# Kernel optimization log

Measured on AMD Instinct MI355X. Metric: run time of the kernel, lower is better.

The kernel has to match this reference:

```python
import jax, jax.numpy as jnp
import numpy as np

T, N, DH, E = 4, 50000, 64, 800000
BN_EPS = 1e-5


def setup_inputs() -> dict:
    key = jax.random.key(0)
    ks = jax.random.split(key, 8)
    node_data = jax.random.normal(ks[0], (T, N, DH), dtype=jnp.float32)
    edge_weight = jax.random.uniform(ks[1], (E,), dtype=jnp.float32)
    W1 = jax.random.normal(ks[2], (DH, 3 * DH), dtype=jnp.float32) * 0.05
    b1 = jax.random.normal(ks[3], (DH,), dtype=jnp.float32) * 0.05
    gamma = jnp.ones((3 * DH,), dtype=jnp.float32)
    beta = jnp.zeros((3 * DH,), dtype=jnp.float32)
    src = jax.random.randint(ks[4], (E,), 0, N)
    dst = jax.random.randint(ks[5], (E,), 0, N)
    return {"node_data": node_data, "edge_weight": edge_weight, "W1": W1,
            "b1": b1, "gamma": gamma, "beta": beta, "src": src, "dst": dst}


def reference(node_data, edge_weight, W1, b1, gamma, beta, src, dst):
    # --- sparse weighted neighbor aggregation (torch.bmm with sparse ew) ---
    # msg[t, e, :] = w_e * x[t, src_e, :]
    msg = node_data[:, src, :] * edge_weight[None, :, None]          # [T, E, dh]
    agg = jnp.zeros((T, N, DH), jnp.float32).at[:, dst, :].add(msg)  # [T, N, dh]
    # Z = torch.sparse.sum(ew, dim=2); Z[Z==0]=1 (degree normalization)
    Z = jnp.zeros((N,), jnp.float32).at[dst].add(edge_weight)
    Z = jnp.where(Z == 0, 1.0, Z)
    avg_neighbor = agg / Z[None, :, None]
    # prev_state: zeros at t=0, shifted node_data otherwise
    prev = jnp.concatenate([jnp.zeros((1, N, DH), jnp.float32), node_data[:-1]], axis=0)
    inp = jnp.concatenate([node_data, prev, avg_neighbor], axis=2).reshape(T * N, 3 * DH)
    # --- ReluFCN with batchnorm (training-mode batch stats, biased var) ---
    mu = jnp.mean(inp, axis=0)
    var = jnp.mean(jnp.square(inp - mu), axis=0)
    xhat = (inp - mu) * jax.lax.rsqrt(var + BN_EPS) * gamma + beta
    out = jax.nn.relu(xhat @ W1.T + b1)
    return out.reshape(T, N, DH)
```

## Files before the change

kernel.cpp:

```cpp
#include <hip/hip_runtime.h>

#define TT 4
#define NN 50000
#define DH 64
#define EE 800000
#define BN_EPS 1e-5f
#define G1 64
#define EB 2048
#define AGG_B 2048
#define AGG_W (AGG_B*4)
#define MAIN_B 768
#define FOLD_B 8
#define CAP 32
#define DSTR 8
#define PASLOT 32
#define OVMAX 256

typedef __attribute__((ext_vector_type(8))) short short8;
typedef __attribute__((ext_vector_type(4))) float floatx4;

#define WS_PA       0
#define WS_PA2      8192
#define WS_PX       16384
#define WS_PX2      81920
#define WS_W1EFF    147456
#define WS_B1EFF    172032
#define WS_OVC      172288
#define WS_OVF      172544
#define WS_DEG      176640
#define WS_PACKED   1776640
#define WS_XB       8176640
#define WS_AVGB     33776640

__device__ __forceinline__ unsigned short f2b(float f) {
    unsigned int u = __float_as_uint(f);
    unsigned int r = (u + 0x7FFFu + ((u >> 16) & 1u)) >> 16;
    return (unsigned short)r;
}
__device__ __forceinline__ float b2f(unsigned short u) {
    return __uint_as_float((unsigned int)u << 16);
}
__device__ __forceinline__ unsigned short f2h(float f) {
    _Float16 h = (_Float16)f;
    unsigned short u; __builtin_memcpy(&u, &h, 2); return u;
}
__device__ __forceinline__ float h2f(unsigned short u) {
    _Float16 h; __builtin_memcpy(&h, &u, 2); return (float)h;
}

__global__ __launch_bounds__(256) void k_prep_stats(
    const float* __restrict__ x, unsigned short* __restrict__ xb,
    float* __restrict__ PX, float* __restrict__ PX2,
    int* __restrict__ deg, int* __restrict__ ovc) {
    int t = blockIdx.y;
    int tid = threadIdx.x;
    int gid = (t * G1 + blockIdx.x) * 256 + tid;
    int4* deg4 = (int4*)deg;
    for (int i = gid; i < NN * DSTR / 4; i += 65536)
        deg4[i] = make_int4(0, 0, 0, 0);
    if (gid == 0) *ovc = 0;

    int g = blockIdx.x * 256 + tid;
    const floatx4* xt = (const floatx4*)(x + (size_t)t * NN * 64);
    float s[4] = {0.f, 0.f, 0.f, 0.f}, s2[4] = {0.f, 0.f, 0.f, 0.f};
    for (int v = g; v < NN * 16; v += G1 * 256) {
        floatx4 d = __builtin_nontemporal_load(&xt[v]);
        ushort4 o;
        o.x = f2b(d.x); o.y = f2b(d.y); o.z = f2b(d.z); o.w = f2b(d.w);
        *(ushort4*)(xb + (size_t)(v >> 4) * 256 + t * 64 + (v & 15) * 4) = o;
        s[0] += d.x; s2[0] += d.x * d.x;
        s[1] += d.y; s2[1] += d.y * d.y;
        s[2] += d.z; s2[2] += d.z * d.z;
        s[3] += d.w; s2[3] += d.w * d.w;
    }
    __shared__ float ls[256 * 4], ls2[256 * 4];
#pragma unroll
    for (int j = 0; j < 4; ++j) { ls[tid * 4 + j] = s[j]; ls2[tid * 4 + j] = s2[j]; }
    __syncthreads();
    if (tid < 64) {
        int g16 = tid >> 2, comp = tid & 3;
        float rs = 0.f, rs2 = 0.f;
#pragma unroll
        for (int k = 0; k < 16; ++k) {
            int j = g16 + 16 * k;
            rs += ls[j * 4 + comp]; rs2 += ls2[j * 4 + comp];
        }
        int slot = (t * G1 + blockIdx.x) * 64 + tid;
        PX[slot] = rs; PX2[slot] = rs2;
    }
}

__global__ __launch_bounds__(256) void k_fillB(
    const int* __restrict__ src, const int* __restrict__ dst,
    const float* __restrict__ ew, int* __restrict__ deg,
    unsigned int* __restrict__ packed, int* __restrict__ ovc,
    int4* __restrict__ ovf, float* __restrict__ PA) {
    int gtid = blockIdx.x * 256 + threadIdx.x;
    if (gtid < 2 * PASLOT * 64) PA[gtid] = 0.f;
    for (int e = gtid; e < EE; e += EB * 256) {
        int d = dst[e];
        int s = src[e];
        float w = ew[e];
        int slot = atomicAdd(&deg[d * DSTR], 1);
        if (slot < CAP) {
            packed[d * CAP + slot] = (unsigned int)s | ((unsigned int)f2h(w) << 16);
        } else {
            int o = atomicAdd(ovc, 1);
            if (o < OVMAX) ovf[o] = make_int4(d, s, __float_as_int(w), 0);
        }
    }
}

__global__ __launch_bounds__(256) void k_agg(
    const unsigned short* __restrict__ xb, const unsigned int* __restrict__ packed,
    const int* __restrict__ deg, const int* __restrict__ ovc,
    const int4* __restrict__ ovf, unsigned short* __restrict__ avgb,
    float* __restrict__ PA, float* __restrict__ PA2) {
    int wv = __builtin_amdgcn_readfirstlane(threadIdx.x >> 6);
    int tid = threadIdx.x;
    int l = tid & 63;
    int wgid = blockIdx.x * 4 + wv;
    const ushort4* xl = (const ushort4*)xb + l;
    int nov = *ovc; nov = nov > OVMAX ? OVMAX : nov;
    float sA[4] = {0.f, 0.f, 0.f, 0.f}, sA2[4] = {0.f, 0.f, 0.f, 0.f};

    for (int n = wgid; n < NN; n += AGG_W) {
        int dg = deg[n * DSTR];
        int cnt = dg < CAP ? dg : CAP;
        const unsigned int* bkt = packed + n * CAP;
        float a0 = 0.f, a1 = 0.f, a2 = 0.f, a3 = 0.f, wsum = 0.f;
        for (int e = 0; e < cnt; e += 8) {
            int rem = cnt - e;
            unsigned int p[8];
#pragma unroll
            for (int j = 0; j < 8; ++j) p[j] = bkt[e + j];
            ushort4 v[8];
#pragma unroll
            for (int j = 0; j < 8; ++j) {
                int sidx = (j < rem) ? (int)(p[j] & 0xFFFFu) : 0;
                v[j] = xl[(size_t)sidx * 64];
            }
#pragma unroll
            for (int j = 0; j < 8; ++j) {
                float w = (j < rem) ? h2f((unsigned short)(p[j] >> 16)) : 0.f;
                wsum += w;
                a0 = fmaf(w, b2f(v[j].x), a0);
                a1 = fmaf(w, b2f(v[j].y), a1);
                a2 = fmaf(w, b2f(v[j].z), a2);
                a3 = fmaf(w, b2f(v[j].w), a3);
            }
        }
        if (dg > CAP) {
            for (int o = 0; o < nov; ++o) {
                int4 E = ovf[o];
                if (E.x == n) {
                    float w = __int_as_float(E.z);
                    ushort4 v = xl[(size_t)E.y * 64];
                    wsum += w;
                    a0 = fmaf(w, b2f(v.x), a0); a1 = fmaf(w, b2f(v.y), a1);
                    a2 = fmaf(w, b2f(v.z), a2); a3 = fmaf(w, b2f(v.w), a3);
                }
            }
        }
        float rz = (wsum == 0.f) ? 1.f : (1.f / wsum);
        ushort4 o;
        o.x = f2b(a0 * rz); o.y = f2b(a1 * rz);
        o.z = f2b(a2 * rz); o.w = f2b(a3 * rz);
        *((ushort4*)avgb + (size_t)n * 64 + l) = o;
        float f0 = b2f(o.x), f1 = b2f(o.y), f2v = b2f(o.z), f3 = b2f(o.w);
        sA[0] += f0; sA2[0] += f0 * f0;
        sA[1] += f1; sA2[1] += f1 * f1;
        sA[2] += f2v; sA2[2] += f2v * f2v;
        sA[3] += f3; sA2[3] += f3 * f3;
    }

    __shared__ float ls[256 * 4], ls2[256 * 4];
#pragma unroll
    for (int j = 0; j < 4; ++j) { ls[tid * 4 + j] = sA[j]; ls2[tid * 4 + j] = sA2[j]; }
    __syncthreads();
    if (tid < 64) {
        int g15 = tid >> 2, j = tid & 3;
        float rs = 0.f, rs2 = 0.f;
#pragma unroll
        for (int k = 0; k < 16; ++k) {
            int st = k * 16 + g15;
            rs += ls[st * 4 + j]; rs2 += ls2[st * 4 + j];
        }
        int slot = (blockIdx.x & (PASLOT - 1)) * 64 + tid;
        atomicAdd(&PA[slot], rs);
        atomicAdd(&PA2[slot], rs2);
    }
}

__global__ __launch_bounds__(256) void k_fold(
    const float* __restrict__ W1, const float* __restrict__ b1,
    const float* __restrict__ gamma, const float* __restrict__ beta,
    const float* __restrict__ PX, const float* __restrict__ PX2,
    const float* __restrict__ PA, const float* __restrict__ PA2,
    unsigned short* __restrict__ W1eff, float* __restrict__ b1eff) {
    __shared__ float spx[4][64], spx2[4][64], spa[64], spa2[64];
    __shared__ float gS[192], hS[192];
    int tid = threadIdx.x;
    int p = tid >> 6, cc = tid & 63;
    float s = 0.f, s2 = 0.f;
    for (int b = 0; b < G1; ++b) {
        int i = (p * G1 + b) * 64 + cc;
        s += PX[i]; s2 += PX2[i];
    }
    spx[p][cc] = s; spx2[p][cc] = s2;
    if (tid < 64) {
        float a = 0.f, a2 = 0.f;
        for (int i = 0; i < PASLOT; ++i) { a += PA[i * 64 + tid]; a2 += PA2[i * 64 + tid]; }
        spa[tid] = a; spa2[tid] = a2;
    }
    __syncthreads();
    const float inv = 1.0f / (float)(TT * NN);
    if (tid < 192) {
        int c = tid;
        float ss, ss2;
        if (c < 64) {
            ss  = spx[0][c] + spx[1][c] + spx[2][c] + spx[3][c];
            ss2 = spx2[0][c] + spx2[1][c] + spx2[2][c] + spx2[3][c];
        } else if (c < 128) {
            int k = c - 64;
            ss  = spx[0][k] + spx[1][k] + spx[2][k];
            ss2 = spx2[0][k] + spx2[1][k] + spx2[2][k];
        } else {
            int k = c - 128;
            ss = spa[k]; ss2 = spa2[k];
        }
        float mu = ss * inv, ex2 = ss2 * inv;
        float var = ex2 - mu * mu;
        float g = gamma[c] / sqrtf(var + BN_EPS);
        gS[c] = g;
        hS[c] = beta[c] - mu * g;
    }
    __syncthreads();
    if (tid < 192) {
        for (int i = blockIdx.x * 192 + tid; i < 64 * 192; i += FOLD_B * 192)
            W1eff[i] = f2b(W1[i] * gS[tid]);
    }
    if (tid < 8) {
        int o = blockIdx.x * 8 + tid;
        float acc = b1[o];
        for (int c = 0; c < 192; ++c) acc += hS[c] * W1[o * 192 + c];
        b1eff[o] = acc;
    }
}

__global__ __launch_bounds__(256, 3) void k_main(
    const unsigned short* __restrict__ xb, const unsigned short* __restrict__ avgb,
    const unsigned short* __restrict__ Wb, const float* __restrict__ bias,
    float* __restrict__ out) {
    int wave = threadIdx.x >> 6;
    int lane = threadIdx.x & 63;
    int m = lane & 15;
    int q = lane >> 4;
    const short8 zf = (short8){0, 0, 0, 0, 0, 0, 0, 0};

    short8 bw[6][4];
#pragma unroll
    for (int kc = 0; kc < 6; ++kc)
#pragma unroll
        for (int ct = 0; ct < 4; ++ct)
            bw[kc][ct] = *(const short8*)(Wb + (size_t)(ct * 16 + m) * 192 + kc * 32 + q * 8);
    float bv[4];
#pragma unroll
    for (int ct = 0; ct < 4; ++ct) bv[ct] = bias[ct * 16 + m];

    for (int tile = blockIdx.x; tile < (TT * NN) / 64; tile += MAIN_B) {
        int r0 = tile * 64 + wave * 16;
        int t = r0 / NN;
        int n0 = r0 - t * NN;
        size_t nb = (size_t)(n0 + m) * 256 + (size_t)t * 64 + q * 8;
        const unsigned short* xrow = xb + nb;
        const unsigned short* arow = avgb + nb;
        bool has_prev = (t >= 1);

        short8 a[6];
        a[0] = *(const short8*)(xrow);
        a[1] = *(const short8*)(xrow + 32);
        a[2] = has_prev ? *(const short8*)(xrow - 64) : zf;
        a[3] = has_prev ? *(const short8*)(xrow - 32) : zf;
        a[4] = *(const short8*)(arow);
        a[5] = *(const short8*)(arow + 32);

        floatx4 acc[4];
#pragma unroll
        for (int ct = 0; ct < 4; ++ct) acc[ct] = (floatx4){0.f, 0.f, 0.f, 0.f};
#pragma unroll
        for (int kc = 0; kc < 6; ++kc)
#pragma unroll
            for (int ct = 0; ct < 4; ++ct)
                acc[ct] = __builtin_amdgcn_mfma_f32_16x16x32_bf16(a[kc], bw[kc][ct], acc[ct], 0, 0, 0);

#pragma unroll
        for (int ct = 0; ct < 4; ++ct)
#pragma unroll
            for (int i = 0; i < 4; ++i) {
                int row = q * 4 + i;
                __builtin_nontemporal_store(fmaxf(acc[ct][i] + bv[ct], 0.f),
                                            &out[(size_t)(r0 + row) * 64 + ct * 16 + m]);
            }
    }
}

extern "C" void kernel_launch(void* const* d_in, const int* in_sizes, int n_in,
                              void* d_out, int out_size, void* d_ws, size_t ws_size,
                              hipStream_t stream) {
    const float* x     = (const float*)d_in[0];
    const float* ew    = (const float*)d_in[1];
    const float* W1    = (const float*)d_in[2];
    const float* b1    = (const float*)d_in[3];
    const float* gamma = (const float*)d_in[4];
    const float* beta  = (const float*)d_in[5];
    const int*   src   = (const int*)d_in[6];
    const int*   dst   = (const int*)d_in[7];
    float* out = (float*)d_out;
    char*  ws  = (char*)d_ws;

    float* PA       = (float*)(ws + WS_PA);
    float* PA2      = (float*)(ws + WS_PA2);
    float* PX       = (float*)(ws + WS_PX);
    float* PX2      = (float*)(ws + WS_PX2);
    unsigned short* W1eff = (unsigned short*)(ws + WS_W1EFF);
    float* b1eff    = (float*)(ws + WS_B1EFF);
    int*   ovc      = (int*)(ws + WS_OVC);
    int4*  ovf      = (int4*)(ws + WS_OVF);
    int*   deg      = (int*)(ws + WS_DEG);
    unsigned int* packed = (unsigned int*)(ws + WS_PACKED);
    unsigned short* xb   = (unsigned short*)(ws + WS_XB);
    unsigned short* avgb = (unsigned short*)(ws + WS_AVGB);

    k_prep_stats<<<dim3(G1, TT), 256, 0, stream>>>(x, xb, PX, PX2, deg, ovc);

    k_fillB<<<EB, 256, 0, stream>>>(src, dst, ew, deg, packed, ovc, ovf, PA);

    k_agg<<<AGG_B, 256, 0, stream>>>(xb, packed, deg, ovc, ovf, avgb, PA, PA2);

    k_fold<<<FOLD_B, 256, 0, stream>>>(W1, b1, gamma, beta, PX, PX2, PA, PA2, W1eff, b1eff);

    k_main<<<MAIN_B, 256, 0, stream>>>(xb, avgb, W1eff, b1eff, out);
}
```

Measured before the change: 275.4 us.

## Split neighbor aggregation into per-timestep launches with lanes spread over edges

Replaces the single aggregation kernel with four launches, one per timestep. Each wave splits its 64 lanes into four edge groups of 16 lanes, each group reading one 128-byte timestep slice, and combines the partial sums with cross-lane shuffles. The aim is to keep a smaller gathered working set (one timestep's rows) resident in cache during each pass. In exchange, the bucket metadata is read four times, there are extra launches and shuffle reductions, and only a quarter of the lanes do the output and statistics work.

```diff
diff --git a/kernel.cpp b/kernel.cpp
--- a/kernel.cpp
+++ b/kernel.cpp
@@ -111,16 +111,18 @@
     }
 }
 
-__global__ __launch_bounds__(256) void k_agg(
+__global__ __launch_bounds__(256) void k_aggT(
     const unsigned short* __restrict__ xb, const unsigned int* __restrict__ packed,
     const int* __restrict__ deg, const int* __restrict__ ovc,
     const int4* __restrict__ ovf, unsigned short* __restrict__ avgb,
-    float* __restrict__ PA, float* __restrict__ PA2) {
+    float* __restrict__ PA, float* __restrict__ PA2, int t) {
     int wv = __builtin_amdgcn_readfirstlane(threadIdx.x >> 6);
     int tid = threadIdx.x;
     int l = tid & 63;
+    int eh = l >> 4;
+    int j = l & 15;
     int wgid = blockIdx.x * 4 + wv;
-    const ushort4* xl = (const ushort4*)xb + l;
+    const ushort4* xq = (const ushort4*)xb + (size_t)t * 16 + j;
     int nov = *ovc; nov = nov > OVMAX ? OVMAX : nov;
     float sA[4] = {0.f, 0.f, 0.f, 0.f}, sA2[4] = {0.f, 0.f, 0.f, 0.f};
 
@@ -133,58 +135,66 @@
             int rem = cnt - e;
             unsigned int p[8];
 #pragma unroll
-            for (int j = 0; j < 8; ++j) p[j] = bkt[e + j];
-            ushort4 v[8];
-#pragma unroll
-            for (int j = 0; j < 8; ++j) {
-                int sidx = (j < rem) ? (int)(p[j] & 0xFFFFu) : 0;
-                v[j] = xl[(size_t)sidx * 64];
-            }
-#pragma unroll
-            for (int j = 0; j < 8; ++j) {
-                float w = (j < rem) ? h2f((unsigned short)(p[j] >> 16)) : 0.f;
-                wsum += w;
-                a0 = fmaf(w, b2f(v[j].x), a0);
-                a1 = fmaf(w, b2f(v[j].y), a1);
-                a2 = fmaf(w, b2f(v[j].z), a2);
-                a3 = fmaf(w, b2f(v[j].w), a3);
-            }
+            for (int q = 0; q < 8; ++q) p[q] = bkt[e + q];
+            unsigned int pe0 = (eh == 0) ? p[0] : (eh == 1) ? p[1] : (eh == 2) ? p[2] : p[3];
+            unsigned int pe1 = (eh == 0) ? p[4] : (eh == 1) ? p[5] : (eh == 2) ? p[6] : p[7];
+            bool ok0 = (eh < rem);
+            bool ok1 = (eh + 4 < rem);
+            int  s0 = ok0 ? (int)(pe0 & 0xFFFFu) : 0;
+            int  s1 = ok1 ? (int)(pe1 & 0xFFFFu) : 0;
+            ushort4 v0 = xq[(size_t)s0 * 64];
+            ushort4 v1 = xq[(size_t)s1 * 64];
+            float w0 = ok0 ? h2f((unsigned short)(pe0 >> 16)) : 0.f;
+            float w1 = ok1 ? h2f((unsigned short)(pe1 >> 16)) : 0.f;
+            wsum += w0 + w1;
+            a0 = fmaf(w0, b2f(v0.x), a0); a0 = fmaf(w1, b2f(v1.x), a0);
+            a1 = fmaf(w0, b2f(v0.y), a1); a1 = fmaf(w1, b2f(v1.y), a1);
+            a2 = fmaf(w0, b2f(v0.z), a2); a2 = fmaf(w1, b2f(v1.z), a2);
+            a3 = fmaf(w0, b2f(v0.w), a3); a3 = fmaf(w1, b2f(v1.w), a3);
         }
         if (dg > CAP) {
             for (int o = 0; o < nov; ++o) {
                 int4 E = ovf[o];
                 if (E.x == n) {
-                    float w = __int_as_float(E.z);
-                    ushort4 v = xl[(size_t)E.y * 64];
+                    float w = (eh == 0) ? __int_as_float(E.z) : 0.f;
+                    ushort4 v = xq[(size_t)E.y * 64];
                     wsum += w;
                     a0 = fmaf(w, b2f(v.x), a0); a1 = fmaf(w, b2f(v.y), a1);
                     a2 = fmaf(w, b2f(v.z), a2); a3 = fmaf(w, b2f(v.w), a3);
                 }
             }
         }
-        float rz = (wsum == 0.f) ? 1.f : (1.f / wsum);
-        ushort4 o;
-        o.x = f2b(a0 * rz); o.y = f2b(a1 * rz);
-        o.z = f2b(a2 * rz); o.w = f2b(a3 * rz);
-        *((ushort4*)avgb + (size_t)n * 64 + l) = o;
-        float f0 = b2f(o.x), f1 = b2f(o.y), f2v = b2f(o.z), f3 = b2f(o.w);
-        sA[0] += f0; sA2[0] += f0 * f0;
-        sA[1] += f1; sA2[1] += f1 * f1;
-        sA[2] += f2v; sA2[2] += f2v * f2v;
-        sA[3] += f3; sA2[3] += f3 * f3;
+        a0 += __shfl_xor(a0, 16); a0 += __shfl_xor(a0, 32);
+        a1 += __shfl_xor(a1, 16); a1 += __shfl_xor(a1, 32);
+        a2 += __shfl_xor(a2, 16); a2 += __shfl_xor(a2, 32);
+        a3 += __shfl_xor(a3, 16); a3 += __shfl_xor(a3, 32);
+        wsum += __shfl_xor(wsum, 16); wsum += __shfl_xor(wsum, 32);
+
+        if (eh == 0) {
+            float rz = (wsum == 0.f) ? 1.f : (1.f / wsum);
+            ushort4 o;
+            o.x = f2b(a0 * rz); o.y = f2b(a1 * rz);
+            o.z = f2b(a2 * rz); o.w = f2b(a3 * rz);
+            *((ushort4*)avgb + (size_t)n * 64 + (size_t)t * 16 + j) = o;
+            float f0 = b2f(o.x), f1 = b2f(o.y), f2v = b2f(o.z), f3 = b2f(o.w);
+            sA[0] += f0; sA2[0] += f0 * f0;
+            sA[1] += f1; sA2[1] += f1 * f1;
+            sA[2] += f2v; sA2[2] += f2v * f2v;
+            sA[3] += f3; sA2[3] += f3 * f3;
+        }
     }
 
     __shared__ float ls[256 * 4], ls2[256 * 4];
 #pragma unroll
-    for (int j = 0; j < 4; ++j) { ls[tid * 4 + j] = sA[j]; ls2[tid * 4 + j] = sA2[j]; }
+    for (int q = 0; q < 4; ++q) { ls[tid * 4 + q] = sA[q]; ls2[tid * 4 + q] = sA2[q]; }
     __syncthreads();
     if (tid < 64) {
-        int g15 = tid >> 2, j = tid & 3;
+        int g15 = tid >> 2, q = tid & 3;
         float rs = 0.f, rs2 = 0.f;
 #pragma unroll
         for (int k = 0; k < 16; ++k) {
             int st = k * 16 + g15;
-            rs += ls[st * 4 + j]; rs2 += ls2[st * 4 + j];
+            rs += ls[st * 4 + q]; rs2 += ls2[st * 4 + q];
         }
         int slot = (blockIdx.x & (PASLOT - 1)) * 64 + tid;
         atomicAdd(&PA[slot], rs);
@@ -336,7 +346,10 @@
 
     k_fillB<<<EB, 256, 0, stream>>>(src, dst, ew, deg, packed, ovc, ovf, PA);
 
-    k_agg<<<AGG_B, 256, 0, stream>>>(xb, packed, deg, ovc, ovf, avgb, PA, PA2);
+    k_aggT<<<AGG_B, 256, 0, stream>>>(xb, packed, deg, ovc, ovf, avgb, PA, PA2, 0);
+    k_aggT<<<AGG_B, 256, 0, stream>>>(xb, packed, deg, ovc, ovf, avgb, PA, PA2, 1);
+    k_aggT<<<AGG_B, 256, 0, stream>>>(xb, packed, deg, ovc, ovf, avgb, PA, PA2, 2);
+    k_aggT<<<AGG_B, 256, 0, stream>>>(xb, packed, deg, ovc, ovf, avgb, PA, PA2, 3);
 
     k_fold<<<FOLD_B, 256, 0, stream>>>(W1, b1, gamma, beta, PX, PX2, PA, PA2, W1eff, b1eff);
 
```

Measured after the change: 300.2 us. 1.09x slower.
